# Optimization experiments

Measured on AMD Instinct MI355X. Metric: run time of the kernel, lower is better.

The kernel has to match this reference:

```python
import jax, jax.numpy as jnp
import numpy as np

N_NODES = 100000
N_EDGES = 1600000
F_IN, HIDDEN, N_CLASS, K = 64, 64, 32, 3
DROPOUT_P = 0.5


def setup_inputs() -> dict:
    key = jax.random.key(0)
    ks = jax.random.split(key, 5)
    x = jax.random.normal(ks[0], (N_NODES, F_IN), dtype=jnp.float32)
    edge_index = jax.random.randint(ks[1], (2, N_EDGES), 0, N_NODES, dtype=jnp.int64)
    W1 = jax.random.normal(ks[2], (K, F_IN, HIDDEN), dtype=jnp.float32) * (1.0 / np.sqrt(F_IN))
    b1 = jnp.zeros((HIDDEN,), dtype=jnp.float32)
    W2 = jax.random.normal(ks[3], (K, HIDDEN, N_CLASS), dtype=jnp.float32) * (1.0 / np.sqrt(HIDDEN))
    b2 = jnp.zeros((N_CLASS,), dtype=jnp.float32)
    return {"x": x, "edge_index": edge_index, "W1": W1, "b1": b1, "W2": W2, "b2": b2}


def _cheb_norm(edge_index, n_nodes):
    # PyG ChebConv sym norm with lambda_max=2: L_hat = -D^{-1/2} A D^{-1/2}
    row, col = edge_index[0], edge_index[1]
    deg = jax.ops.segment_sum(jnp.ones_like(row, dtype=jnp.float32), row, num_segments=n_nodes)
    dinv = jnp.where(deg > 0, jax.lax.rsqrt(jnp.maximum(deg, 1.0)), 0.0)
    return -(dinv[row] * dinv[col])  # [E]


def _cheb_conv(x, row, col, norm, W, b):
    # Chebyshev recursion: Tx0=x, Tx1=L_hat x, Tx_k = 2 L_hat Tx_{k-1} - Tx_{k-2}
    def prop(h):
        return jax.ops.segment_sum(norm[:, None] * h[col], row, num_segments=h.shape[0])
    Tx0 = x
    out = Tx0 @ W[0]
    Tx1 = prop(Tx0)
    out = out + Tx1 @ W[1]
    for k in range(2, W.shape[0]):
        Tx2 = 2.0 * prop(Tx1) - Tx0
        out = out + Tx2 @ W[k]
        Tx0, Tx1 = Tx1, Tx2
    return out + b


def reference(x, edge_index, W1, b1, W2, b2):
    row, col = edge_index[0], edge_index[1]
    norm = _cheb_norm(edge_index, x.shape[0])
    h = jax.nn.relu(_cheb_conv(x, row, col, norm, W1, b1))
    # dropout (training=True) with fixed key, inverted scaling
    keep = jax.random.bernoulli(jax.random.key(42), 1.0 - DROPOUT_P, h.shape)
    h = jnp.where(keep, h / (1.0 - DROPOUT_P), 0.0)
    out = _cheb_conv(h, row, col, norm, W2, b2)
    return jax.nn.log_softmax(out, axis=-1)
```

## Files before the change

kernel.cpp:

```cpp
#include <hip/hip_runtime.h>


static constexpr int BLK = 256;
static constexpr int SCAN_CHUNK = 256;
static constexpr int ROWB = 256;
static constexpr int RB_SHIFT = 8;
static constexpr int BCAP = 6144;
static constexpr int CHUNK = 8192;

typedef _Float16 f16x8 __attribute__((ext_vector_type(8)));
typedef float f32x4 __attribute__((ext_vector_type(4)));

__device__ __forceinline__ unsigned rotl32(unsigned x, int r) {
    return (x << r) | (x >> (32 - r));
}

__device__ __forceinline__ unsigned tf_word(unsigned i) {
    const unsigned ks0 = 0u;
    const unsigned ks1 = 42u;
    const unsigned ks2 = 0u ^ 42u ^ 0x1BD11BDAu;
    unsigned x0 = 0u + ks0;
    unsigned x1 = i + ks1;
#define TF_RND(r) { x0 += x1; x1 = rotl32(x1, (r)); x1 ^= x0; }
    TF_RND(13) TF_RND(15) TF_RND(26) TF_RND(6)
    x0 += ks1; x1 += ks2 + 1u;
    TF_RND(17) TF_RND(29) TF_RND(16) TF_RND(24)
    x0 += ks2; x1 += ks0 + 2u;
    TF_RND(13) TF_RND(15) TF_RND(26) TF_RND(6)
    x0 += ks0; x1 += ks1 + 3u;
    TF_RND(17) TF_RND(29) TF_RND(16) TF_RND(24)
    x0 += ks1; x1 += ks2 + 4u;
    TF_RND(13) TF_RND(15) TF_RND(26) TF_RND(6)
    x0 += ks2; x1 += ks0 + 5u;
#undef TF_RND
    return x0 ^ x1;
}

__device__ __forceinline__ float lo16(unsigned u) {
    union { unsigned x; float f; } c; c.x = u << 16; return c.f;
}
__device__ __forceinline__ float hi16(unsigned u) {
    union { unsigned x; float f; } c; c.x = u & 0xFFFF0000u; return c.f;
}
__device__ __forceinline__ unsigned short f2b(float f) {
    union { float f; unsigned u; } c; c.f = f;
    unsigned r = (c.u + 0x7FFFu + ((c.u >> 16) & 1u)) >> 16;
    return (unsigned short)r;
}
__device__ __forceinline__ unsigned pack2(float a, float b) {
    return (unsigned)f2b(a) | ((unsigned)f2b(b) << 16);
}

__global__ void k_detect(const int* __restrict__ ei, int* __restrict__ flags) {
    __shared__ int cnt_nz;
    int t = threadIdx.x;
    if (t == 0) cnt_nz = 0;
    __syncthreads();
    if (ei[2 * t + 1] != 0) atomicAdd(&cnt_nz, 1);
    __syncthreads();
    if (t == 0) flags[0] = (cnt_nz == 0) ? 1 : 0;
}

__global__ void __launch_bounds__(256) k_bin(const int* __restrict__ ei, int E,
                                             const int* __restrict__ flags,
                                             int* __restrict__ bcnt,
                                             unsigned* __restrict__ bdata, int NB) {
    __shared__ unsigned sval[CHUNK];
    __shared__ unsigned short sbkt[CHUNK];
    __shared__ int h[512], ex[512], cur[512], basep[512];
    int t = threadIdx.x;
    int start = blockIdx.x * CHUNK;
    int lim = min(CHUNK, E - start);
    bool i64 = flags[0] != 0;
    h[t] = 0; h[t + 256] = 0;
    __syncthreads();
    unsigned vv[32];
    unsigned short bb_[32];
#pragma unroll
    for (int k = 0; k < 32; ++k) {
        int idx = k * 256 + t;
        int e = start + idx;
        if (idx < lim) {
            int r, c;
            if (i64) { r = ei[2 * e]; c = ei[2 * (E + e)]; }
            else     { r = ei[e];     c = ei[E + e]; }
            int b = r >> RB_SHIFT;
            vv[k] = ((unsigned)(r & (ROWB - 1)) << 17) | (unsigned)c;
            bb_[k] = (unsigned short)b;
            atomicAdd(&h[b], 1);
        } else {
            bb_[k] = 0xFFFF;
        }
    }
    __syncthreads();
    int i0 = t, i1 = t + 256;
    ex[i0] = h[i0]; ex[i1] = h[i1];
    __syncthreads();
    for (int off = 1; off < 512; off <<= 1) {
        int v0 = (i0 >= off) ? ex[i0 - off] : 0;
        int v1 = (i1 >= off) ? ex[i1 - off] : 0;
        __syncthreads();
        ex[i0] += v0; ex[i1] += v1;
        __syncthreads();
    }
    int e0 = ex[i0] - h[i0], e1 = ex[i1] - h[i1];
    __syncthreads();
    ex[i0] = e0; cur[i0] = e0;
    ex[i1] = e1; cur[i1] = e1;
    if (i0 < NB && h[i0] > 0) basep[i0] = atomicAdd(&bcnt[i0], h[i0]);
    if (i1 < NB && h[i1] > 0) basep[i1] = atomicAdd(&bcnt[i1], h[i1]);
    __syncthreads();
#pragma unroll
    for (int k = 0; k < 32; ++k) {
        if (bb_[k] != 0xFFFF) {
            int p = atomicAdd(&cur[bb_[k]], 1);
            sval[p] = vv[k];
            sbkt[p] = bb_[k];
        }
    }
    __syncthreads();
    for (int i = t; i < lim; i += 256) {
        int b = sbkt[i];
        int gpos = basep[b] + (i - ex[b]);
        if (gpos < BCAP) bdata[(size_t)b * BCAP + gpos] = sval[i];
    }
}

__global__ void __launch_bounds__(256) k_hist2(const unsigned* __restrict__ bdata,
                                               const int* __restrict__ bcnt,
                                               int N, int* __restrict__ deg,
                                               float* __restrict__ dinv) {
    __shared__ int h[ROWB];
    int t = threadIdx.x, b = blockIdx.x;
    h[t] = 0;
    __syncthreads();
    int cnt = min(bcnt[b], BCAP);
    for (int i = t; i < cnt; i += 256)
        atomicAdd(&h[bdata[(size_t)b * BCAP + i] >> 17], 1);
    __syncthreads();
    int r = b * ROWB + t;
    if (r < N) {
        int d = h[t];
        deg[r] = d;
        dinv[r] = (d > 0) ? rsqrtf((float)d) : 0.0f;
    }
}

__global__ void k_scanA(const int* __restrict__ deg, int N, int* __restrict__ blk_sum) {
    __shared__ int lds[SCAN_CHUNK];
    int i = blockIdx.x * SCAN_CHUNK + threadIdx.x;
    int v = (i < N) ? deg[i] : 0;
    lds[threadIdx.x] = v;
    __syncthreads();
    for (int off = SCAN_CHUNK / 2; off > 0; off >>= 1) {
        if (threadIdx.x < off) lds[threadIdx.x] += lds[threadIdx.x + off];
        __syncthreads();
    }
    if (threadIdx.x == 0) blk_sum[blockIdx.x] = lds[0];
}

__global__ void k_scanB(int* __restrict__ blk_sum, int nb) {
    __shared__ int lds[1024];
    int t = threadIdx.x;
    int v = (t < nb) ? blk_sum[t] : 0;
    lds[t] = v;
    __syncthreads();
    for (int off = 1; off < 1024; off <<= 1) {
        int val = (t >= off) ? lds[t - off] : 0;
        __syncthreads();
        lds[t] += val;
        __syncthreads();
    }
    if (t < nb) blk_sum[t] = lds[t] - v;
}

__global__ void k_scanC(const int* __restrict__ deg, int N, int E,
                        const int* __restrict__ blk_sum, int* __restrict__ row_ptr) {
    __shared__ int lds[SCAN_CHUNK];
    int t = threadIdx.x;
    int i = blockIdx.x * SCAN_CHUNK + t;
    int v = (i < N) ? deg[i] : 0;
    lds[t] = v;
    __syncthreads();
    for (int off = 1; off < SCAN_CHUNK; off <<= 1) {
        int val = (t >= off) ? lds[t - off] : 0;
        __syncthreads();
        lds[t] += val;
        __syncthreads();
    }
    if (i < N) row_ptr[i] = blk_sum[blockIdx.x] + lds[t] - v;
    if (blockIdx.x == gridDim.x - 1 && t == SCAN_CHUNK - 1) row_ptr[N] = E;
}

__global__ void __launch_bounds__(256) k_place(const unsigned* __restrict__ bdata,
                                               const int* __restrict__ bcnt,
                                               const int* __restrict__ row_ptr,
                                               int N, int* __restrict__ sdst) {
    __shared__ int cur[ROWB];
    __shared__ int staged[BCAP];
    int t = threadIdx.x, b = blockIdx.x;
    int r0 = b * ROWB;
    int rbase = row_ptr[r0];
    int r = r0 + t;
    cur[t] = (r < N) ? (row_ptr[r] - rbase) : 0;
    __syncthreads();
    int cnt = min(bcnt[b], BCAP);
    for (int i = t; i < cnt; i += 256) {
        unsigned val = bdata[(size_t)b * BCAP + i];
        int p = atomicAdd(&cur[val >> 17], 1);
        staged[p] = (int)(val & 0x1FFFFu);
    }
    __syncthreads();
    for (int i = t; i < cnt; i += 256) sdst[rbase + i] = staged[i];
}

__global__ void k_wprep(const float* __restrict__ W1, const float* __restrict__ W2,
                        unsigned short* __restrict__ wt1,
                        unsigned short* __restrict__ wt2) {
    int idx = blockIdx.x * 256 + threadIdx.x;
    if (idx < 12288) {
        int c = idx >> 6, r6 = idx & 63;
        int slot = (r6 >> 3) ^ (c & 7);
        int k = slot * 8 + (r6 & 7);
        float v;
        if (c < 64)       v = W1[k * 64 + c] - W1[8192 + k * 64 + c];
        else if (c < 128) v = W1[4096 + k * 64 + (c - 64)];
        else              v = W1[8192 + k * 64 + (c - 128)];
        union { _Float16 h; unsigned short u; } cv; cv.h = (_Float16)v;
        wt1[idx] = cv.u;
    } else {
        int j = idx - 12288;
        int c = j >> 6, r6 = j & 63;
        int slot = (r6 >> 3) ^ (c & 7);
        int k = slot * 8 + (r6 & 7);
        float v;
        if (c < 32)      v = W2[k * 32 + c] - W2[4096 + k * 32 + c];
        else if (c < 64) v = W2[2048 + k * 32 + (c - 32)];
        else             v = W2[4096 + k * 32 + (c - 64)];
        union { _Float16 h; unsigned short u; } cv; cv.h = (_Float16)v;
        wt2[j] = cv.u;
    }
}

__global__ void __launch_bounds__(512) k_dense3(const float* __restrict__ x,
                                                const unsigned short* __restrict__ wt1,
                                                const float* __restrict__ b1,
                                                const float* __restrict__ dinv,
                                                int N,
                                                unsigned short* __restrict__ B16,
                                                unsigned short* __restrict__ C16,
                                                float* __restrict__ D) {
    __shared__ unsigned short lds[20480] __attribute__((aligned(16)));
    __shared__ float sb[64];
    int t = threadIdx.x;
    int v0 = blockIdx.x * 128;
    {
        const uint4* src = (const uint4*)wt1;
        uint4* dst = (uint4*)&lds[8192];
        for (int i = t; i < 1536; i += 512) dst[i] = src[i];
    }
    if (t < 64) sb[t] = b1[t];
    {
        int row = t >> 2, c0 = (t & 3) << 4;
        int v = min(v0 + row, N - 1);
        const float* xp = x + (size_t)v * 64 + c0;
        float4 f0 = *(const float4*)xp;
        float4 f1 = *(const float4*)(xp + 4);
        float4 f2 = *(const float4*)(xp + 8);
        float4 f3 = *(const float4*)(xp + 12);
        int key = row & 7;
        int s0 = c0 >> 3;
        f16x8 h0, h1;
        h0[0] = (_Float16)f0.x; h0[1] = (_Float16)f0.y;
        h0[2] = (_Float16)f0.z; h0[3] = (_Float16)f0.w;
        h0[4] = (_Float16)f1.x; h0[5] = (_Float16)f1.y;
        h0[6] = (_Float16)f1.z; h0[7] = (_Float16)f1.w;
        h1[0] = (_Float16)f2.x; h1[1] = (_Float16)f2.y;
        h1[2] = (_Float16)f2.z; h1[3] = (_Float16)f2.w;
        h1[4] = (_Float16)f3.x; h1[5] = (_Float16)f3.y;
        h1[6] = (_Float16)f3.z; h1[7] = (_Float16)f3.w;
        *(f16x8*)&lds[row * 64 + ((s0 ^ key) << 3)] = h0;
        *(f16x8*)&lds[row * 64 + (((s0 + 1) ^ key) << 3)] = h1;
    }
    __syncthreads();

    int w = t >> 6, l = t & 63;
    int lr = l & 15, lk = l >> 4;
    int key = lr & 7;
    int arow = w * 16 + lr;
    f16x8 a0 = *(const f16x8*)&lds[arow * 64 + (((0 + lk) ^ key) << 3)];
    f16x8 a1 = *(const f16x8*)&lds[arow * 64 + (((4 + lk) ^ key) << 3)];
    f32x4 acc[12];
#pragma unroll
    for (int i = 0; i < 12; ++i) acc[i] = (f32x4){0.0f, 0.0f, 0.0f, 0.0f};
#pragma unroll
    for (int nt = 0; nt < 12; ++nt) {
        int bc = nt * 16 + lr;
        const unsigned short* wb = &lds[8192 + bc * 64];
        f16x8 b0 = *(const f16x8*)&wb[((0 + lk) ^ key) << 3];
        f16x8 b1v = *(const f16x8*)&wb[((4 + lk) ^ key) << 3];
        acc[nt] = __builtin_amdgcn_mfma_f32_16x16x32_f16(a0, b0, acc[nt], 0, 0, 0);
        acc[nt] = __builtin_amdgcn_mfma_f32_16x16x32_f16(a1, b1v, acc[nt], 0, 0, 0);
    }
    float4 dv4 = *(const float4*)&dinv[v0 + w * 16 + lk * 4];
    float dsc[4] = {dv4.x, dv4.y, dv4.z, dv4.w};
#pragma unroll
    for (int nt = 0; nt < 4; ++nt) {
        int col = nt * 16 + lr;
        float bv = sb[col];
#pragma unroll
        for (int r = 0; r < 4; ++r) {
            int v = v0 + w * 16 + lk * 4 + r;
            if (v < N) D[(size_t)v * 64 + col] = acc[nt][r] + bv;
        }
    }
    __syncthreads();
#pragma unroll
    for (int nt = 4; nt < 8; ++nt) {
        int col = (nt - 4) * 16 + lr;
#pragma unroll
        for (int r = 0; r < 4; ++r) {
            int vloc = w * 16 + lk * 4 + r;
            lds[vloc * 128 + col] = f2b(acc[nt][r]);
        }
    }
#pragma unroll
    for (int nt = 8; nt < 12; ++nt) {
        int col = (nt - 4) * 16 + lr;
#pragma unroll
        for (int r = 0; r < 4; ++r) {
            int vloc = w * 16 + lk * 4 + r;
            lds[vloc * 128 + col] = f2b(acc[nt][r] * dsc[r]);
        }
    }
    __syncthreads();
#pragma unroll
    for (int q = 0; q < 4; ++q) {
        int i = q * 512 + t;
        int row = i >> 4, ch = i & 15;
        int v = v0 + row;
        if (v < N) {
            uint4 val = *(const uint4*)&lds[i * 8];
            unsigned short* dst = (ch < 8)
                ? (B16 + (size_t)v * 64 + ch * 8)
                : (C16 + (size_t)v * 64 + (ch - 8) * 8);
            *(uint4*)dst = val;
        }
    }
}

__global__ void __launch_bounds__(512) k_dense3b(const unsigned short* __restrict__ wt2,
                                                 const float* __restrict__ dinv,
                                                 int N,
                                                 unsigned short* __restrict__ B16,
                                                 const float* __restrict__ C,
                                                 float* __restrict__ P0,
                                                 float* __restrict__ P1) {
    __shared__ unsigned short lds[14336] __attribute__((aligned(16)));
    int t = threadIdx.x;
    int v0 = blockIdx.x * 128;
    {
        const uint4* src = (const uint4*)wt2;
        uint4* dst = (uint4*)&lds[8192];
        for (int i = t; i < 768; i += 512) dst[i] = src[i];
    }
    {
        int row = t >> 2, c0 = (t & 3) << 4;
        int v = min(v0 + row, N - 1);
        const float* xp = C + (size_t)v * 64 + c0;
        float4 f0 = *(const float4*)xp;
        float4 f1 = *(const float4*)(xp + 4);
        float4 f2 = *(const float4*)(xp + 8);
        float4 f3 = *(const float4*)(xp + 12);
        int key = row & 7;
        int s0 = c0 >> 3;
        f16x8 h0, h1;
        h0[0] = (_Float16)f0.x; h0[1] = (_Float16)f0.y;
        h0[2] = (_Float16)f0.z; h0[3] = (_Float16)f0.w;
        h0[4] = (_Float16)f1.x; h0[5] = (_Float16)f1.y;
        h0[6] = (_Float16)f1.z; h0[7] = (_Float16)f1.w;
        h1[0] = (_Float16)f2.x; h1[1] = (_Float16)f2.y;
        h1[2] = (_Float16)f2.z; h1[3] = (_Float16)f2.w;
        h1[4] = (_Float16)f3.x; h1[5] = (_Float16)f3.y;
        h1[6] = (_Float16)f3.z; h1[7] = (_Float16)f3.w;
        *(f16x8*)&lds[row * 64 + ((s0 ^ key) << 3)] = h0;
        *(f16x8*)&lds[row * 64 + (((s0 + 1) ^ key) << 3)] = h1;
    }
    __syncthreads();

    int w = t >> 6, l = t & 63;
    int lr = l & 15, lk = l >> 4;
    int key = lr & 7;
    int arow = w * 16 + lr;
    f16x8 a0 = *(const f16x8*)&lds[arow * 64 + (((0 + lk) ^ key) << 3)];
    f16x8 a1 = *(const f16x8*)&lds[arow * 64 + (((4 + lk) ^ key) << 3)];
    f32x4 acc[6];
#pragma unroll
    for (int i = 0; i < 6; ++i) acc[i] = (f32x4){0.0f, 0.0f, 0.0f, 0.0f};
#pragma unroll
    for (int nt = 0; nt < 6; ++nt) {
        int bc = nt * 16 + lr;
        const unsigned short* wb = &lds[8192 + bc * 64];
        f16x8 b0 = *(const f16x8*)&wb[((0 + lk) ^ key) << 3];
        f16x8 b1v = *(const f16x8*)&wb[((4 + lk) ^ key) << 3];
        acc[nt] = __builtin_amdgcn_mfma_f32_16x16x32_f16(a0, b0, acc[nt], 0, 0, 0);
        acc[nt] = __builtin_amdgcn_mfma_f32_16x16x32_f16(a1, b1v, acc[nt], 0, 0, 0);
    }
    float4 dv4 = *(const float4*)&dinv[v0 + w * 16 + lk * 4];
    float dsc[4] = {dv4.x, dv4.y, dv4.z, dv4.w};
#pragma unroll
    for (int nt = 0; nt < 4; ++nt) {
        int col = (nt & 1) * 16 + lr;
        float* dst = (nt < 2) ? P0 : P1;
#pragma unroll
        for (int r = 0; r < 4; ++r) {
            int v = v0 + w * 16 + lk * 4 + r;
            if (v < N) dst[(size_t)v * 32 + col] = acc[nt][r];
        }
    }
    __syncthreads();
#pragma unroll
    for (int nt = 4; nt < 6; ++nt) {
        int col = (nt - 4) * 16 + lr;
#pragma unroll
        for (int r = 0; r < 4; ++r) {
            int vloc = w * 16 + lk * 4 + r;
            lds[vloc * 32 + col] = f2b(acc[nt][r] * dsc[r]);
        }
    }
    __syncthreads();
    {
        int i = t;
        int row = i >> 2, ch = i & 3;
        int v = v0 + row;
        if (v < N) {
            uint4 val = *(const uint4*)&lds[i * 8];
            *(uint4*)(B16 + (size_t)v * 32 + ch * 8) = val;
        }
    }
}

template <int PITCH>
__device__ __forceinline__ void gatherH(const unsigned short* __restrict__ src,
                                        const int* __restrict__ sdst,
                                        int beg, int end, int grp, int fl,
                                        float a[8]) {
    constexpr int NG = 32 / (PITCH / 8);
#pragma unroll
    for (int q = 0; q < 8; ++q) a[q] = 0.0f;
    int e = beg + grp;
    for (; e + NG < end; e += 2 * NG) {
        int c0 = sdst[e];
        int c1 = sdst[e + NG];
        uint4 r0 = *(const uint4*)(src + (size_t)c0 * PITCH + 8 * fl);
        uint4 r1 = *(const uint4*)(src + (size_t)c1 * PITCH + 8 * fl);
        a[0] += lo16(r0.x); a[1] += hi16(r0.x);
        a[2] += lo16(r0.y); a[3] += hi16(r0.y);
        a[4] += lo16(r0.z); a[5] += hi16(r0.z);
        a[6] += lo16(r0.w); a[7] += hi16(r0.w);
        a[0] += lo16(r1.x); a[1] += hi16(r1.x);
        a[2] += lo16(r1.y); a[3] += hi16(r1.y);
        a[4] += lo16(r1.z); a[5] += hi16(r1.z);
        a[6] += lo16(r1.w); a[7] += hi16(r1.w);
    }
    if (e < end) {
        int c = sdst[e];
        uint4 r = *(const uint4*)(src + (size_t)c * PITCH + 8 * fl);
        a[0] += lo16(r.x); a[1] += hi16(r.x);
        a[2] += lo16(r.y); a[3] += hi16(r.y);
        a[4] += lo16(r.z); a[5] += hi16(r.z);
        a[6] += lo16(r.w); a[7] += hi16(r.w);
    }
#pragma unroll
    for (int m = PITCH / 8; m < 32; m <<= 1) {
#pragma unroll
        for (int q = 0; q < 8; ++q) a[q] += __shfl_xor(a[q], m);
    }
}

__global__ void __launch_bounds__(BLK) k_gath1(const unsigned short* __restrict__ C16,
                                               unsigned short* __restrict__ B16,
                                               const float* __restrict__ dinv,
                                               const int* __restrict__ row_ptr,
                                               const int* __restrict__ sdst,
                                               int N) {
    int v = blockIdx.x * 8 + (threadIdx.x >> 5);
    if (v >= N) return;
    int hl = threadIdx.x & 31;
    int grp = hl >> 3, fl = hl & 7;
    float a[8];
    gatherH<64>(C16, sdst, row_ptr[v], row_ptr[v + 1], grp, fl, a);
    if (grp == 0) {
        float di = dinv[v];
        float dv = -2.0f * di;
        unsigned short* p = B16 + (size_t)v * 64 + 8 * fl;
        uint4 b = *(const uint4*)p;
        float q0 = di * fmaf(dv, a[0], lo16(b.x)), q1 = di * fmaf(dv, a[1], hi16(b.x));
        float q2 = di * fmaf(dv, a[2], lo16(b.y)), q3 = di * fmaf(dv, a[3], hi16(b.y));
        float q4 = di * fmaf(dv, a[4], lo16(b.z)), q5 = di * fmaf(dv, a[5], hi16(b.z));
        float q6 = di * fmaf(dv, a[6], lo16(b.w)), q7 = di * fmaf(dv, a[7], hi16(b.w));
        uint4 o;
        o.x = pack2(q0, q1); o.y = pack2(q2, q3);
        o.z = pack2(q4, q5); o.w = pack2(q6, q7);
        *(uint4*)p = o;
    }
}

__global__ void __launch_bounds__(BLK) k_gath2(const float* __restrict__ D,
                                               const unsigned short* __restrict__ B16,
                                               float* __restrict__ C,
                                               const float* __restrict__ dinv,
                                               const int* __restrict__ row_ptr,
                                               const int* __restrict__ sdst,
                                               int N) {
    int v = blockIdx.x * 8 + (threadIdx.x >> 5);
    if (v >= N) return;
    int lane = threadIdx.x & 63;
    int hl = lane & 31;
    int grp = hl >> 3, fl = hl & 7;
    float a[8];
    gatherH<64>(B16, sdst, row_ptr[v], row_ptr[v + 1], grp, fl, a);
    unsigned wA = tf_word((unsigned)v * 64u + 2u * (unsigned)hl);
    unsigned wB = tf_word((unsigned)v * 64u + 2u * (unsigned)hl + 1u);
    int base = (lane & 32) + 4 * fl;
    unsigned ww[8];
#pragma unroll
    for (int k = 0; k < 8; ++k) ww[k] = __shfl((k & 1) ? wB : wA, base + (k >> 1));
    if (grp == 0) {
        float dv = -dinv[v];
        const float* dp = D + (size_t)v * 64 + 8 * fl;
        float4 dA = *(const float4*)dp;
        float4 dB = *(const float4*)(dp + 4);
        float o[8];
        o[0] = fmaxf(fmaf(dv, a[0], dA.x), 0.0f);
        o[1] = fmaxf(fmaf(dv, a[1], dA.y), 0.0f);
        o[2] = fmaxf(fmaf(dv, a[2], dA.z), 0.0f);
        o[3] = fmaxf(fmaf(dv, a[3], dA.w), 0.0f);
        o[4] = fmaxf(fmaf(dv, a[4], dB.x), 0.0f);
        o[5] = fmaxf(fmaf(dv, a[5], dB.y), 0.0f);
        o[6] = fmaxf(fmaf(dv, a[6], dB.z), 0.0f);
        o[7] = fmaxf(fmaf(dv, a[7], dB.w), 0.0f);
#pragma unroll
        for (int k = 0; k < 8; ++k)
            o[k] = (ww[k] & 0x80000000u) ? 0.0f : o[k] * 2.0f;
        float* cp = C + (size_t)v * 64 + 8 * fl;
        *(float4*)cp = make_float4(o[0], o[1], o[2], o[3]);
        *(float4*)(cp + 4) = make_float4(o[4], o[5], o[6], o[7]);
    }
}

__global__ void __launch_bounds__(BLK) k_gath3(const unsigned short* __restrict__ B16,
                                               const float* __restrict__ P1,
                                               unsigned short* __restrict__ R16,
                                               const float* __restrict__ dinv,
                                               const int* __restrict__ row_ptr,
                                               const int* __restrict__ sdst,
                                               int N) {
    int v = blockIdx.x * 8 + (threadIdx.x >> 5);
    if (v >= N) return;
    int hl = threadIdx.x & 31;
    int grp = hl >> 2, fl = hl & 3;
    float a[8];
    gatherH<32>(B16, sdst, row_ptr[v], row_ptr[v + 1], grp, fl, a);
    if (grp == 0) {
        float di = dinv[v];
        float dv = -2.0f * di;
        const float* dp = P1 + (size_t)v * 32 + 8 * fl;
        float4 dA = *(const float4*)dp;
        float4 dB = *(const float4*)(dp + 4);
        uint4 o;
        o.x = pack2(di * fmaf(dv, a[0], dA.x), di * fmaf(dv, a[1], dA.y));
        o.y = pack2(di * fmaf(dv, a[2], dA.z), di * fmaf(dv, a[3], dA.w));
        o.z = pack2(di * fmaf(dv, a[4], dB.x), di * fmaf(dv, a[5], dB.y));
        o.w = pack2(di * fmaf(dv, a[6], dB.z), di * fmaf(dv, a[7], dB.w));
        *(uint4*)(R16 + (size_t)v * 32 + 8 * fl) = o;
    }
}

__global__ void __launch_bounds__(BLK) k_gath4(const unsigned short* __restrict__ R16,
                                               const float* __restrict__ P0,
                                               const float* __restrict__ dinv,
                                               const int* __restrict__ row_ptr,
                                               const int* __restrict__ sdst,
                                               const float* __restrict__ b2,
                                               int N, float* __restrict__ out) {
    int v = blockIdx.x * 8 + (threadIdx.x >> 5);
    if (v >= N) return;
    int hl = threadIdx.x & 31;
    int grp = hl >> 2, fl = hl & 3;
    float a[8];
    gatherH<32>(R16, sdst, row_ptr[v], row_ptr[v + 1], grp, fl, a);
    float dv = -dinv[v];
    const float* dp = P0 + (size_t)v * 32 + 8 * fl;
    float4 dA = *(const float4*)dp;
    float4 dB = *(const float4*)(dp + 4);
    const float* bp = b2 + 8 * fl;
    float4 bA = *(const float4*)bp;
    float4 bB = *(const float4*)(bp + 4);
    float o[8];
    o[0] = fmaf(dv, a[0], dA.x + bA.x);
    o[1] = fmaf(dv, a[1], dA.y + bA.y);
    o[2] = fmaf(dv, a[2], dA.z + bA.z);
    o[3] = fmaf(dv, a[3], dA.w + bA.w);
    o[4] = fmaf(dv, a[4], dB.x + bB.x);
    o[5] = fmaf(dv, a[5], dB.y + bB.y);
    o[6] = fmaf(dv, a[6], dB.z + bB.z);
    o[7] = fmaf(dv, a[7], dB.w + bB.w);
    float m = o[0];
#pragma unroll
    for (int k = 1; k < 8; ++k) m = fmaxf(m, o[k]);
    m = fmaxf(m, __shfl_xor(m, 1));
    m = fmaxf(m, __shfl_xor(m, 2));
    float s = 0.0f;
#pragma unroll
    for (int k = 0; k < 8; ++k) s += __expf(o[k] - m);
    s += __shfl_xor(s, 1);
    s += __shfl_xor(s, 2);
    float lse = m + __logf(s);
    if (grp == 0) {
        float* op = out + (size_t)v * 32 + 8 * fl;
        *(float4*)op = make_float4(o[0] - lse, o[1] - lse, o[2] - lse, o[3] - lse);
        *(float4*)(op + 4) = make_float4(o[4] - lse, o[5] - lse, o[6] - lse, o[7] - lse);
    }
}

extern "C" void kernel_launch(void* const* d_in, const int* in_sizes, int n_in,
                              void* d_out, int out_size, void* d_ws, size_t ws_size,
                              hipStream_t stream) {
    const float* x  = (const float*)d_in[0];
    const int* ei   = (const int*)d_in[1];
    const float* W1 = (const float*)d_in[2];
    const float* b1 = (const float*)d_in[3];
    const float* W2 = (const float*)d_in[4];
    const float* b2 = (const float*)d_in[5];
    float* out = (float*)d_out;

    const int N = in_sizes[0] / 64;
    const int E = in_sizes[1] / 2;
    const int NB = (N + ROWB - 1) >> RB_SHIFT;

    char* ws = (char*)d_ws;
    size_t off = 0;
    auto alloc = [&](size_t bytes) -> void* {
        void* p = ws + off;
        off = (off + bytes + 511) & ~(size_t)511;
        return p;
    };
    int*      flags   = (int*)alloc(16);
    int*      deg     = (int*)alloc((size_t)N * 4);
    float*    dinv    = (float*)alloc((size_t)N * 4);
    int*      row_ptr = (int*)alloc(((size_t)N + 1) * 4);
    int*      blk_sum = (int*)alloc(4096);
    int*      bcnt    = (int*)alloc((size_t)NB * 4);
    size_t dbytes = (size_t)N * 64 * 4;
    size_t bdbytes = (size_t)NB * BCAP * 4;
    unsigned* bdata = (unsigned*)alloc(dbytes > bdbytes ? dbytes : bdbytes);
    float*    D     = (float*)bdata;
    float*    P0    = (float*)bdata;
    float*    P1    = P0 + (size_t)N * 32;
    int*      sdst  = (int*)alloc((size_t)E * 4);
    float*    C     = (float*)alloc((size_t)N * 64 * 4);
    unsigned short* B16 = (unsigned short*)alloc((size_t)N * 64 * 2);
    unsigned short* C16 = (unsigned short*)alloc((size_t)N * 64 * 2);
    unsigned short* R16 = C16;
    unsigned short* wt1 = (unsigned short*)alloc(12288 * 2);
    unsigned short* wt2 = (unsigned short*)alloc(6144 * 2);

    hipMemsetAsync(bcnt, 0, (size_t)NB * 4, stream);

    const int gW8 = (N + 7) / 8;
    const int gDM = (N + 127) / 128;
    const int nb = (N + SCAN_CHUNK - 1) / SCAN_CHUNK;
    const int gBin = (E + CHUNK - 1) / CHUNK;

    k_wprep<<<72, 256, 0, stream>>>(W1, W2, wt1, wt2);
    k_detect<<<1, 256, 0, stream>>>(ei, flags);
    k_bin<<<gBin, 256, 0, stream>>>(ei, E, flags, bcnt, bdata, NB);
    k_hist2<<<NB, 256, 0, stream>>>(bdata, bcnt, N, deg, dinv);
    k_scanA<<<nb, SCAN_CHUNK, 0, stream>>>(deg, N, blk_sum);
    k_scanB<<<1, 1024, 0, stream>>>(blk_sum, nb);
    k_scanC<<<nb, SCAN_CHUNK, 0, stream>>>(deg, N, E, blk_sum, row_ptr);
    k_place<<<NB, 256, 0, stream>>>(bdata, bcnt, row_ptr, N, sdst);

    k_dense3<<<gDM, 512, 0, stream>>>(x, wt1, b1, dinv, N, B16, C16, D);
    k_gath1<<<gW8, BLK, 0, stream>>>(C16, B16, dinv, row_ptr, sdst, N);
    k_gath2<<<gW8, BLK, 0, stream>>>(D, B16, C, dinv, row_ptr, sdst, N);

    k_dense3b<<<gDM, 512, 0, stream>>>(wt2, dinv, N, B16, C, P0, P1);
    k_gath3<<<gW8, BLK, 0, stream>>>(B16, P1, R16, dinv, row_ptr, sdst, N);
    k_gath4<<<gW8, BLK, 0, stream>>>(R16, P0, dinv, row_ptr, sdst, b2, N, out);
}
```

Before: 282.7 us.

## Switch intermediates from bf16/fp32 to fp16 and precompute dropout bitmask

```diff
diff --git a/kernel.cpp b/kernel.cpp
--- a/kernel.cpp
+++ b/kernel.cpp
@@ -9,6 +9,7 @@
 static constexpr int CHUNK = 8192;
 
 typedef _Float16 f16x8 __attribute__((ext_vector_type(8)));
+typedef _Float16 f16x2 __attribute__((ext_vector_type(2)));
 typedef float f32x4 __attribute__((ext_vector_type(4)));
 
 __device__ __forceinline__ unsigned rotl32(unsigned x, int r) {
@@ -36,19 +37,13 @@
     return x0 ^ x1;
 }
 
-__device__ __forceinline__ float lo16(unsigned u) {
-    union { unsigned x; float f; } c; c.x = u << 16; return c.f;
-}
-__device__ __forceinline__ float hi16(unsigned u) {
-    union { unsigned x; float f; } c; c.x = u & 0xFFFF0000u; return c.f;
-}
-__device__ __forceinline__ unsigned short f2b(float f) {
-    union { float f; unsigned u; } c; c.f = f;
-    unsigned r = (c.u + 0x7FFFu + ((c.u >> 16) & 1u)) >> 16;
-    return (unsigned short)r;
-}
-__device__ __forceinline__ unsigned pack2(float a, float b) {
-    return (unsigned)f2b(a) | ((unsigned)f2b(b) << 16);
+__device__ __forceinline__ unsigned short f2h(float f) {
+    union { _Float16 h; unsigned short u; } c; c.h = (_Float16)f; return c.u;
+}
+__device__ __forceinline__ unsigned pack2h(float a, float b) {
+    union { f16x2 h; unsigned u; } c;
+    c.h[0] = (_Float16)a; c.h[1] = (_Float16)b;
+    return c.u;
 }
 
 __global__ void k_detect(const int* __restrict__ ei, int* __restrict__ flags) {
@@ -59,6 +54,13 @@
     if (ei[2 * t + 1] != 0) atomicAdd(&cnt_nz, 1);
     __syncthreads();
     if (t == 0) flags[0] = (cnt_nz == 0) ? 1 : 0;
+}
+
+__global__ void __launch_bounds__(256) k_drop(int NW, unsigned long long* __restrict__ dmask) {
+    int idx = blockIdx.x * 256 + threadIdx.x;
+    unsigned word = (idx < NW) ? tf_word((unsigned)idx) : 0u;
+    unsigned long long bal = __ballot(word >> 31);
+    if ((threadIdx.x & 63) == 0 && idx < NW) dmask[idx >> 6] = bal;
 }
 
 __global__ void __launch_bounds__(256) k_bin(const int* __restrict__ ei, int E,
@@ -226,8 +228,7 @@
         if (c < 64)       v = W1[k * 64 + c] - W1[8192 + k * 64 + c];
         else if (c < 128) v = W1[4096 + k * 64 + (c - 64)];
         else              v = W1[8192 + k * 64 + (c - 128)];
-        union { _Float16 h; unsigned short u; } cv; cv.h = (_Float16)v;
-        wt1[idx] = cv.u;
+        wt1[idx] = f2h(v);
     } else {
         int j = idx - 12288;
         int c = j >> 6, r6 = j & 63;
@@ -237,8 +238,7 @@
         if (c < 32)      v = W2[k * 32 + c] - W2[4096 + k * 32 + c];
         else if (c < 64) v = W2[2048 + k * 32 + (c - 32)];
         else             v = W2[4096 + k * 32 + (c - 64)];
-        union { _Float16 h; unsigned short u; } cv; cv.h = (_Float16)v;
-        wt2[j] = cv.u;
+        wt2[j] = f2h(v);
     }
 }
 
@@ -249,7 +249,7 @@
                                                 int N,
                                                 unsigned short* __restrict__ B16,
                                                 unsigned short* __restrict__ C16,
-                                                float* __restrict__ D) {
+                                                unsigned short* __restrict__ D16) {
     __shared__ unsigned short lds[20480] __attribute__((aligned(16)));
     __shared__ float sb[64];
     int t = threadIdx.x;
@@ -304,15 +304,24 @@
     }
     float4 dv4 = *(const float4*)&dinv[v0 + w * 16 + lk * 4];
     float dsc[4] = {dv4.x, dv4.y, dv4.z, dv4.w};
+    __syncthreads();
 #pragma unroll
     for (int nt = 0; nt < 4; ++nt) {
         int col = nt * 16 + lr;
         float bv = sb[col];
 #pragma unroll
         for (int r = 0; r < 4; ++r) {
-            int v = v0 + w * 16 + lk * 4 + r;
-            if (v < N) D[(size_t)v * 64 + col] = acc[nt][r] + bv;
-        }
+            int vloc = w * 16 + lk * 4 + r;
+            lds[vloc * 64 + col] = f2h(acc[nt][r] + bv);
+        }
+    }
+    __syncthreads();
+#pragma unroll
+    for (int q = 0; q < 2; ++q) {
+        int i = q * 512 + t;
+        int row = i >> 3, ch = i & 7;
+        int v = v0 + row;
+        if (v < N) *(uint4*)(D16 + (size_t)v * 64 + ch * 8) = ((const uint4*)lds)[i];
     }
     __syncthreads();
 #pragma unroll
@@ -321,7 +330,7 @@
 #pragma unroll
         for (int r = 0; r < 4; ++r) {
             int vloc = w * 16 + lk * 4 + r;
-            lds[vloc * 128 + col] = f2b(acc[nt][r]);
+            lds[vloc * 128 + col] = f2h(acc[nt][r]);
         }
     }
 #pragma unroll
@@ -330,7 +339,7 @@
 #pragma unroll
         for (int r = 0; r < 4; ++r) {
             int vloc = w * 16 + lk * 4 + r;
-            lds[vloc * 128 + col] = f2b(acc[nt][r] * dsc[r]);
+            lds[vloc * 128 + col] = f2h(acc[nt][r] * dsc[r]);
         }
     }
     __syncthreads();
@@ -353,9 +362,9 @@
                                                  const float* __restrict__ dinv,
                                                  int N,
                                                  unsigned short* __restrict__ B16,
-                                                 const float* __restrict__ C,
+                                                 const unsigned short* __restrict__ C16h,
                                                  float* __restrict__ P0,
-                                                 float* __restrict__ P1) {
+                                                 unsigned short* __restrict__ P1h) {
     __shared__ unsigned short lds[14336] __attribute__((aligned(16)));
     int t = threadIdx.x;
     int v0 = blockIdx.x * 128;
@@ -365,26 +374,14 @@
         for (int i = t; i < 768; i += 512) dst[i] = src[i];
     }
     {
-        int row = t >> 2, c0 = (t & 3) << 4;
+        int row = t >> 2, s0 = (t & 3) * 2;
         int v = min(v0 + row, N - 1);
-        const float* xp = C + (size_t)v * 64 + c0;
-        float4 f0 = *(const float4*)xp;
-        float4 f1 = *(const float4*)(xp + 4);
-        float4 f2 = *(const float4*)(xp + 8);
-        float4 f3 = *(const float4*)(xp + 12);
+        const uint4* cp = (const uint4*)(C16h + (size_t)v * 64);
+        uint4 u0 = cp[s0];
+        uint4 u1 = cp[s0 + 1];
         int key = row & 7;
-        int s0 = c0 >> 3;
-        f16x8 h0, h1;
-        h0[0] = (_Float16)f0.x; h0[1] = (_Float16)f0.y;
-        h0[2] = (_Float16)f0.z; h0[3] = (_Float16)f0.w;
-        h0[4] = (_Float16)f1.x; h0[5] = (_Float16)f1.y;
-        h0[6] = (_Float16)f1.z; h0[7] = (_Float16)f1.w;
-        h1[0] = (_Float16)f2.x; h1[1] = (_Float16)f2.y;
-        h1[2] = (_Float16)f2.z; h1[3] = (_Float16)f2.w;
-        h1[4] = (_Float16)f3.x; h1[5] = (_Float16)f3.y;
-        h1[6] = (_Float16)f3.z; h1[7] = (_Float16)f3.w;
-        *(f16x8*)&lds[row * 64 + ((s0 ^ key) << 3)] = h0;
-        *(f16x8*)&lds[row * 64 + (((s0 + 1) ^ key) << 3)] = h1;
+        *(uint4*)&lds[row * 64 + ((s0 ^ key) << 3)] = u0;
+        *(uint4*)&lds[row * 64 + (((s0 + 1) ^ key) << 3)] = u1;
     }
     __syncthreads();
 
@@ -409,33 +406,45 @@
     float4 dv4 = *(const float4*)&dinv[v0 + w * 16 + lk * 4];
     float dsc[4] = {dv4.x, dv4.y, dv4.z, dv4.w};
 #pragma unroll
-    for (int nt = 0; nt < 4; ++nt) {
-        int col = (nt & 1) * 16 + lr;
-        float* dst = (nt < 2) ? P0 : P1;
+    for (int nt = 0; nt < 2; ++nt) {
+        int col = nt * 16 + lr;
 #pragma unroll
         for (int r = 0; r < 4; ++r) {
             int v = v0 + w * 16 + lk * 4 + r;
-            if (v < N) dst[(size_t)v * 32 + col] = acc[nt][r];
-        }
-    }
-    __syncthreads();
-#pragma unroll
-    for (int nt = 4; nt < 6; ++nt) {
-        int col = (nt - 4) * 16 + lr;
+            if (v < N) P0[(size_t)v * 32 + col] = acc[nt][r];
+        }
+    }
+    __syncthreads();
+#pragma unroll
+    for (int nt = 2; nt < 4; ++nt) {
+        int col = (nt - 2) * 16 + lr;
 #pragma unroll
         for (int r = 0; r < 4; ++r) {
             int vloc = w * 16 + lk * 4 + r;
-            lds[vloc * 32 + col] = f2b(acc[nt][r] * dsc[r]);
-        }
-    }
-    __syncthreads();
-    {
-        int i = t;
-        int row = i >> 2, ch = i & 3;
+            lds[vloc * 64 + col] = f2h(acc[nt][r]);
+        }
+    }
+#pragma unroll
+    for (int nt = 4; nt < 6; ++nt) {
+        int col = (nt - 2) * 16 + lr;
+#pragma unroll
+        for (int r = 0; r < 4; ++r) {
+            int vloc = w * 16 + lk * 4 + r;
+            lds[vloc * 64 + col] = f2h(acc[nt][r] * dsc[r]);
+        }
+    }
+    __syncthreads();
+#pragma unroll
+    for (int q = 0; q < 2; ++q) {
+        int i = q * 512 + t;
+        int row = i >> 3, ch = i & 7;
         int v = v0 + row;
         if (v < N) {
-            uint4 val = *(const uint4*)&lds[i * 8];
-            *(uint4*)(B16 + (size_t)v * 32 + ch * 8) = val;
+            uint4 val = ((const uint4*)lds)[i];
+            unsigned short* dst = (ch < 4)
+                ? (P1h + (size_t)v * 32 + ch * 8)
+                : (B16 + (size_t)v * 32 + (ch - 4) * 8);
+            *(uint4*)dst = val;
         }
     }
 }
@@ -446,36 +455,33 @@
                                         int beg, int end, int grp, int fl,
                                         float a[8]) {
     constexpr int NG = 32 / (PITCH / 8);
-#pragma unroll
-    for (int q = 0; q < 8; ++q) a[q] = 0.0f;
+    f16x8 acc;
+#pragma unroll
+    for (int q = 0; q < 8; ++q) acc[q] = (_Float16)0;
     int e = beg + grp;
     for (; e + NG < end; e += 2 * NG) {
         int c0 = sdst[e];
         int c1 = sdst[e + NG];
-        uint4 r0 = *(const uint4*)(src + (size_t)c0 * PITCH + 8 * fl);
-        uint4 r1 = *(const uint4*)(src + (size_t)c1 * PITCH + 8 * fl);
-        a[0] += lo16(r0.x); a[1] += hi16(r0.x);
-        a[2] += lo16(r0.y); a[3] += hi16(r0.y);
-        a[4] += lo16(r0.z); a[5] += hi16(r0.z);
-        a[6] += lo16(r0.w); a[7] += hi16(r0.w);
-        a[0] += lo16(r1.x); a[1] += hi16(r1.x);
-        a[2] += lo16(r1.y); a[3] += hi16(r1.y);
-        a[4] += lo16(r1.z); a[5] += hi16(r1.z);
-        a[6] += lo16(r1.w); a[7] += hi16(r1.w);
+        f16x8 r0 = *(const f16x8*)(src + (size_t)c0 * PITCH + 8 * fl);
+        f16x8 r1 = *(const f16x8*)(src + (size_t)c1 * PITCH + 8 * fl);
+        acc = acc + r0;
+        acc = acc + r1;
     }
     if (e < end) {
         int c = sdst[e];
-        uint4 r = *(const uint4*)(src + (size_t)c * PITCH + 8 * fl);
-        a[0] += lo16(r.x); a[1] += hi16(r.x);
-        a[2] += lo16(r.y); a[3] += hi16(r.y);
-        a[4] += lo16(r.z); a[5] += hi16(r.z);
-        a[6] += lo16(r.w); a[7] += hi16(r.w);
+        f16x8 r = *(const f16x8*)(src + (size_t)c * PITCH + 8 * fl);
+        acc = acc + r;
     }
 #pragma unroll
     for (int m = PITCH / 8; m < 32; m <<= 1) {
-#pragma unroll
-        for (int q = 0; q < 8; ++q) a[q] += __shfl_xor(a[q], m);
-    }
+        union { f16x8 h; int i4[4]; } u;
+        u.h = acc;
+#pragma unroll
+        for (int q = 0; q < 4; ++q) u.i4[q] = __shfl_xor(u.i4[q], m);
+        acc = acc + u.h;
+    }
+#pragma unroll
+    for (int q = 0; q < 8; ++q) a[q] = (float)acc[q];
 }
 
 __global__ void __launch_bounds__(BLK) k_gath1(const unsigned short* __restrict__ C16,
@@ -494,63 +500,50 @@
         float di = dinv[v];
         float dv = -2.0f * di;
         unsigned short* p = B16 + (size_t)v * 64 + 8 * fl;
-        uint4 b = *(const uint4*)p;
-        float q0 = di * fmaf(dv, a[0], lo16(b.x)), q1 = di * fmaf(dv, a[1], hi16(b.x));
-        float q2 = di * fmaf(dv, a[2], lo16(b.y)), q3 = di * fmaf(dv, a[3], hi16(b.y));
-        float q4 = di * fmaf(dv, a[4], lo16(b.z)), q5 = di * fmaf(dv, a[5], hi16(b.z));
-        float q6 = di * fmaf(dv, a[6], lo16(b.w)), q7 = di * fmaf(dv, a[7], hi16(b.w));
+        f16x8 b = *(const f16x8*)p;
         uint4 o;
-        o.x = pack2(q0, q1); o.y = pack2(q2, q3);
-        o.z = pack2(q4, q5); o.w = pack2(q6, q7);
+        o.x = pack2h(di * fmaf(dv, a[0], (float)b[0]), di * fmaf(dv, a[1], (float)b[1]));
+        o.y = pack2h(di * fmaf(dv, a[2], (float)b[2]), di * fmaf(dv, a[3], (float)b[3]));
+        o.z = pack2h(di * fmaf(dv, a[4], (float)b[4]), di * fmaf(dv, a[5], (float)b[5]));
+        o.w = pack2h(di * fmaf(dv, a[6], (float)b[6]), di * fmaf(dv, a[7], (float)b[7]));
         *(uint4*)p = o;
     }
 }
 
-__global__ void __launch_bounds__(BLK) k_gath2(const float* __restrict__ D,
+__global__ void __launch_bounds__(BLK) k_gath2(const unsigned short* __restrict__ D16,
                                                const unsigned short* __restrict__ B16,
-                                               float* __restrict__ C,
+                                               unsigned short* __restrict__ C16h,
+                                               const unsigned long long* __restrict__ dmask,
                                                const float* __restrict__ dinv,
                                                const int* __restrict__ row_ptr,
                                                const int* __restrict__ sdst,
                                                int N) {
     int v = blockIdx.x * 8 + (threadIdx.x >> 5);
     if (v >= N) return;
-    int lane = threadIdx.x & 63;
-    int hl = lane & 31;
+    int hl = threadIdx.x & 31;
     int grp = hl >> 3, fl = hl & 7;
     float a[8];
     gatherH<64>(B16, sdst, row_ptr[v], row_ptr[v + 1], grp, fl, a);
-    unsigned wA = tf_word((unsigned)v * 64u + 2u * (unsigned)hl);
-    unsigned wB = tf_word((unsigned)v * 64u + 2u * (unsigned)hl + 1u);
-    int base = (lane & 32) + 4 * fl;
-    unsigned ww[8];
-#pragma unroll
-    for (int k = 0; k < 8; ++k) ww[k] = __shfl((k & 1) ? wB : wA, base + (k >> 1));
     if (grp == 0) {
+        unsigned long long dm = dmask[v] >> (8 * fl);
         float dv = -dinv[v];
-        const float* dp = D + (size_t)v * 64 + 8 * fl;
-        float4 dA = *(const float4*)dp;
-        float4 dB = *(const float4*)(dp + 4);
+        f16x8 d = *(const f16x8*)(D16 + (size_t)v * 64 + 8 * fl);
         float o[8];
-        o[0] = fmaxf(fmaf(dv, a[0], dA.x), 0.0f);
-        o[1] = fmaxf(fmaf(dv, a[1], dA.y), 0.0f);
-        o[2] = fmaxf(fmaf(dv, a[2], dA.z), 0.0f);
-        o[3] = fmaxf(fmaf(dv, a[3], dA.w), 0.0f);
-        o[4] = fmaxf(fmaf(dv, a[4], dB.x), 0.0f);
-        o[5] = fmaxf(fmaf(dv, a[5], dB.y), 0.0f);
-        o[6] = fmaxf(fmaf(dv, a[6], dB.z), 0.0f);
-        o[7] = fmaxf(fmaf(dv, a[7], dB.w), 0.0f);
 #pragma unroll
         for (int k = 0; k < 8; ++k)
-            o[k] = (ww[k] & 0x80000000u) ? 0.0f : o[k] * 2.0f;
-        float* cp = C + (size_t)v * 64 + 8 * fl;
-        *(float4*)cp = make_float4(o[0], o[1], o[2], o[3]);
-        *(float4*)(cp + 4) = make_float4(o[4], o[5], o[6], o[7]);
+            o[k] = fmaxf(fmaf(dv, a[k], (float)d[k]), 0.0f);
+#pragma unroll
+        for (int k = 0; k < 8; ++k)
+            o[k] = ((dm >> k) & 1ull) ? 0.0f : o[k] * 2.0f;
+        uint4 oo;
+        oo.x = pack2h(o[0], o[1]); oo.y = pack2h(o[2], o[3]);
+        oo.z = pack2h(o[4], o[5]); oo.w = pack2h(o[6], o[7]);
+        *(uint4*)(C16h + (size_t)v * 64 + 8 * fl) = oo;
     }
 }
 
 __global__ void __launch_bounds__(BLK) k_gath3(const unsigned short* __restrict__ B16,
-                                               const float* __restrict__ P1,
+                                               const unsigned short* __restrict__ P1h,
                                                unsigned short* __restrict__ R16,
                                                const float* __restrict__ dinv,
                                                const int* __restrict__ row_ptr,
@@ -565,14 +558,12 @@
     if (grp == 0) {
         float di = dinv[v];
         float dv = -2.0f * di;
-        const float* dp = P1 + (size_t)v * 32 + 8 * fl;
-        float4 dA = *(const float4*)dp;
-        float4 dB = *(const float4*)(dp + 4);
+        f16x8 d = *(const f16x8*)(P1h + (size_t)v * 32 + 8 * fl);
         uint4 o;
-        o.x = pack2(di * fmaf(dv, a[0], dA.x), di * fmaf(dv, a[1], dA.y));
-        o.y = pack2(di * fmaf(dv, a[2], dA.z), di * fmaf(dv, a[3], dA.w));
-        o.z = pack2(di * fmaf(dv, a[4], dB.x), di * fmaf(dv, a[5], dB.y));
-        o.w = pack2(di * fmaf(dv, a[6], dB.z), di * fmaf(dv, a[7], dB.w));
+        o.x = pack2h(di * fmaf(dv, a[0], (float)d[0]), di * fmaf(dv, a[1], (float)d[1]));
+        o.y = pack2h(di * fmaf(dv, a[2], (float)d[2]), di * fmaf(dv, a[3], (float)d[3]));
+        o.z = pack2h(di * fmaf(dv, a[4], (float)d[4]), di * fmaf(dv, a[5], (float)d[5]));
+        o.w = pack2h(di * fmaf(dv, a[6], (float)d[6]), di * fmaf(dv, a[7], (float)d[7]));
         *(uint4*)(R16 + (size_t)v * 32 + 8 * fl) = o;
     }
 }
@@ -655,14 +646,15 @@
     size_t dbytes = (size_t)N * 64 * 4;
     size_t bdbytes = (size_t)NB * BCAP * 4;
     unsigned* bdata = (unsigned*)alloc(dbytes > bdbytes ? dbytes : bdbytes);
-    float*    D     = (float*)bdata;
+    unsigned short* D16 = (unsigned short*)bdata;
     float*    P0    = (float*)bdata;
-    float*    P1    = P0 + (size_t)N * 32;
+    unsigned short* P1h = (unsigned short*)((char*)bdata + (size_t)N * 32 * 4);
     int*      sdst  = (int*)alloc((size_t)E * 4);
-    float*    C     = (float*)alloc((size_t)N * 64 * 4);
+    unsigned short* C16h = (unsigned short*)alloc((size_t)N * 64 * 2);
     unsigned short* B16 = (unsigned short*)alloc((size_t)N * 64 * 2);
     unsigned short* C16 = (unsigned short*)alloc((size_t)N * 64 * 2);
     unsigned short* R16 = C16;
+    unsigned long long* dmask = (unsigned long long*)alloc((size_t)N * 8);
     unsigned short* wt1 = (unsigned short*)alloc(12288 * 2);
     unsigned short* wt2 = (unsigned short*)alloc(6144 * 2);
 
@@ -672,8 +664,10 @@
     const int gDM = (N + 127) / 128;
     const int nb = (N + SCAN_CHUNK - 1) / SCAN_CHUNK;
     const int gBin = (E + CHUNK - 1) / CHUNK;
+    const int gDrop = (N * 64 + 255) / 256;
 
     k_wprep<<<72, 256, 0, stream>>>(W1, W2, wt1, wt2);
+    k_drop<<<gDrop, 256, 0, stream>>>(N * 64, dmask);
     k_detect<<<1, 256, 0, stream>>>(ei, flags);
     k_bin<<<gBin, 256, 0, stream>>>(ei, E, flags, bcnt, bdata, NB);
     k_hist2<<<NB, 256, 0, stream>>>(bdata, bcnt, N, deg, dinv);
@@ -682,11 +676,11 @@
     k_scanC<<<nb, SCAN_CHUNK, 0, stream>>>(deg, N, E, blk_sum, row_ptr);
     k_place<<<NB, 256, 0, stream>>>(bdata, bcnt, row_ptr, N, sdst);
 
-    k_dense3<<<gDM, 512, 0, stream>>>(x, wt1, b1, dinv, N, B16, C16, D);
+    k_dense3<<<gDM, 512, 0, stream>>>(x, wt1, b1, dinv, N, B16, C16, D16);
     k_gath1<<<gW8, BLK, 0, stream>>>(C16, B16, dinv, row_ptr, sdst, N);
-    k_gath2<<<gW8, BLK, 0, stream>>>(D, B16, C, dinv, row_ptr, sdst, N);
-
-    k_dense3b<<<gDM, 512, 0, stream>>>(wt2, dinv, N, B16, C, P0, P1);
-    k_gath3<<<gW8, BLK, 0, stream>>>(B16, P1, R16, dinv, row_ptr, sdst, N);
+    k_gath2<<<gW8, BLK, 0, stream>>>(D16, B16, C16h, dmask, dinv, row_ptr, sdst, N);
+
+    k_dense3b<<<gDM, 512, 0, stream>>>(wt2, dinv, N, B16, C16h, P0, P1h);
+    k_gath3<<<gW8, BLK, 0, stream>>>(B16, P1h, R16, dinv, row_ptr, sdst, N);
     k_gath4<<<gW8, BLK, 0, stream>>>(R16, P0, dinv, row_ptr, sdst, b2, N, out);
 }
```

After: 284.7 us. No clear change (+0.7%).
